# Optimization experiments

Hardware: AMD Instinct MI355X
Metric: run time of the kernel (lower is better)

Reference implementation:

```python
import jax, jax.numpy as jnp
import numpy as np

EPS = 1e-9
# i = 7,6,...,-1 use exp_factor = -(4**i); i = -2 uses 0.0 (matches torch's reversed(range(-2,8)))
EXP_FACTORS = np.array([-(4.0 ** i) for i in range(7, -2, -1)] + [0.0], dtype=np.float32)


def setup_inputs() -> dict:
    key = jax.random.key(0)
    k1, k2 = jax.random.split(key)
    B, N, D = 16, 2048, 3
    preds = jax.random.normal(k1, (B, N, D), dtype=jnp.float32)
    labels = jax.random.normal(k2, (B, N, D), dtype=jnp.float32)
    return {"preds": preds, "labels": labels}


def _pairwise_dist(p1, p2):
    # ||p1||^2 + ||p2||^2 - 2 p1 . p2  -> [B, N, N]
    p1n = jnp.sum(p1 * p1, axis=-1)[..., :, None]
    p2n = jnp.sum(p2 * p2, axis=-1)[..., None, :]
    return p1n + p2n - 2.0 * jnp.einsum('bnd,bmd->bnm', p1, p2)


def _approx_match(pwdist):
    B, N, _ = pwdist.shape
    match0 = jnp.zeros_like(pwdist)
    cost0 = jnp.ones((B, 1, N), dtype=pwdist.dtype)      # per-target remaining capacity
    curr0 = jnp.ones((B, N, 1), dtype=pwdist.dtype)      # per-source remaining currency

    def step(carry, ef):
        match, cost, currency = carry
        bids = jnp.exp(ef * pwdist) * cost
        bids = bids * currency / (jnp.sum(bids, axis=1, keepdims=True) + EPS)
        bid_wt = jnp.minimum(cost / (jnp.sum(bids, axis=1, keepdims=True) + EPS), 1.0)
        bids = bids * bid_wt
        match = match + bids
        cost = jnp.maximum(cost - jnp.sum(bids, axis=1, keepdims=True), 0.0)
        currency = jnp.maximum(currency - jnp.sum(bids, axis=2, keepdims=True), 0.0)
        return (match, cost, currency), None

    (match, _, _), _ = jax.lax.scan(step, (match0, cost0, curr0), jnp.asarray(EXP_FACTORS))
    return match


def reference(preds, labels):
    pwdist = _pairwise_dist(preds, labels)
    match = _approx_match(pwdist)
    return jnp.sum(match * pwdist)
```

## Files before the change

### kernel.cpp

```cpp
#include <hip/hip_runtime.h>
#include <cstddef>

#define BB    16
#define NN    2048
#define BN    (BB * NN)
#define EPSF  1e-9f
#define TPB   512
#define CPT   2
#define SPLIT 16
#define TILE  128
#define CHUNK 1024
#define K9C   4

typedef float v2f __attribute__((ext_vector_type(2)));
typedef float v4f __attribute__((ext_vector_type(4)));

extern "C" __device__ float __ocml_native_exp2_f32(float);
__device__ __forceinline__ float fast_exp2(float x) {
#if __has_builtin(__builtin_amdgcn_exp2f)
    return __builtin_amdgcn_exp2f(x);
#else
    return __ocml_native_exp2_f32(x);
#endif
}

__device__ __forceinline__ v2f pk_fma(v2f a, v2f b, v2f c) {
    v2f d;
    asm("v_pk_fma_f32 %0, %1, %2, %3" : "=v"(d) : "v"(a), "v"(b), "v"(c));
    return d;
}
__device__ __forceinline__ v2f pk_add(v2f a, v2f b) {
    v2f d;
    asm("v_pk_add_f32 %0, %1, %2" : "=v"(d) : "v"(a), "v"(b));
    return d;
}
__device__ __forceinline__ v2f pk_mul(v2f a, v2f b) {
    v2f d;
    asm("v_pk_mul_f32 %0, %1, %2" : "=v"(d) : "v"(a), "v"(b));
    return d;
}

__device__ __forceinline__ float block_sum(float v, int t, float* tmp8) {
#pragma unroll
    for (int o = 32; o > 0; o >>= 1) v += __shfl_down(v, o, 64);
    __syncthreads();
    if ((t & 63) == 0) tmp8[t >> 6] = v;
    __syncthreads();
    float s = 0.0f;
#pragma unroll
    for (int w = 0; w < TPB / 64; w++) s += tmp8[w];
    return s;
}

__global__ __launch_bounds__(TPB, 4) void passA(
    const float* __restrict__ preds, const float* __restrict__ labels,
    const float* __restrict__ curprev, float* __restrict__ curout,
    const float* __restrict__ RSprev, const float* __restrict__ RRprev,
    float* __restrict__ RSz, float* __restrict__ RRz,
    float* __restrict__ Sacc, float* __restrict__ Tacc,
    float* __restrict__ out, float c1, int k)
{
    __shared__ v4f s_pa[TILE / 2];
    __shared__ v4f s_pb[TILE / 2];
    __shared__ v2f s_cu2[TILE / 2];
    __shared__ float s_red[2];
    int blk = blockIdx.x;
    int split = blk & 15, mc = (blk >> 4) & 1, b = blk >> 5;
    int t = threadIdx.x;
    int base = b * NN;

    if (t < TILE) {
        int idx = base + split * TILE + t;
        const float* p = preds + (size_t)idx * 3;
        float px = p[0], py = p[1], pz = p[2];
        float pn = px * px + py * py + pz * pz;
        float cu, contrib = 0.0f;
        if (k == 0) cu = 1.0f;
        else {
            float cup = curprev[idx], rs = RSprev[idx], rr = RRprev[idx];
            contrib = cup * rr;
            cu = fmaxf(cup * (1.0f - rs), 0.0f);
        }
        int h = t >> 1, par = t & 1;
        float* pa = (float*)&s_pa[h];
        float* pb = (float*)&s_pb[h];
        pa[par] = px; pa[2 + par] = py;
        pb[par] = pz; pb[2 + par] = c1 * pn;
        ((float*)s_cu2)[t] = cu;
        if (mc == 0) {
            curout[idx] = cu;
            RSz[idx] = 0.0f; RRz[idx] = 0.0f;
        }
        if (k > 0 && mc == 0) {
#pragma unroll
            for (int o = 32; o > 0; o >>= 1) contrib += __shfl_down(contrib, o, 64);
            if ((t & 63) == 0) s_red[t >> 6] = contrib;
        }
    }

    int m0 = mc * CHUNK + t;
    v2f gx2[CPT], gy2[CPT], gz2[CPT], am2[CPT], Sa2[CPT], Ta2[CPT];
    float n2c1 = -2.0f * c1;
#pragma unroll
    for (int c = 0; c < CPT; c++) {
        int m = m0 + c * TPB;
        const float* l = labels + (size_t)(base + m) * 3;
        float lx = l[0], ly = l[1], lz = l[2];
        float gx = n2c1 * lx, gy = n2c1 * ly, gz = n2c1 * lz;
        float am = c1 * (lx * lx + ly * ly + lz * lz);
        gx2[c] = (v2f){gx, gx}; gy2[c] = (v2f){gy, gy}; gz2[c] = (v2f){gz, gz};
        am2[c] = (v2f){am, am};
        Sa2[c] = (v2f){0.0f, 0.0f}; Ta2[c] = (v2f){0.0f, 0.0f};
    }
    __syncthreads();
    if (k > 0 && mc == 0 && t == 0) atomicAdd(out, s_red[0] + s_red[1]);

#pragma unroll 4
    for (int h = 0; h < TILE / 2; h++) {
        v4f A1 = s_pa[h];
        v4f A2 = s_pb[h];
        v2f cu2 = s_cu2[h];
#pragma unroll
        for (int c = 0; c < CPT; c++) {
            v2f seed = pk_add(A2.zw, am2[c]);
            v2f arg = pk_fma(A1.xy, gx2[c],
                      pk_fma(A1.zw, gy2[c],
                      pk_fma(A2.xy, gz2[c], seed)));
            v2f e2;
            e2.x = fast_exp2(arg.x);
            e2.y = fast_exp2(arg.y);
            Sa2[c] = pk_add(Sa2[c], e2);
            Ta2[c] = pk_fma(e2, cu2, Ta2[c]);
        }
    }
#pragma unroll
    for (int c = 0; c < CPT; c++) {
        int idx = base + m0 + c * TPB;
        atomicAdd(&Sacc[idx], Sa2[c].x + Sa2[c].y);
        atomicAdd(&Tacc[idx], Ta2[c].x + Ta2[c].y);
    }
}

__global__ __launch_bounds__(TPB, 4) void passB(
    const float* __restrict__ preds, const float* __restrict__ labels,
    const float* __restrict__ Sread, const float* __restrict__ Tread,
    const float* __restrict__ costprev, float* __restrict__ costout,
    float* __restrict__ Sz, float* __restrict__ Tz,
    float* __restrict__ RSacc, float* __restrict__ RRacc,
    float c1, float invc1, int k)
{
    __shared__ v4f s_la[TILE / 2];
    __shared__ v4f s_lb[TILE / 2];
    __shared__ v2f s_cc2[TILE / 2];
    int blk = blockIdx.x;
    int split = blk & 15, nc = (blk >> 4) & 1, b = blk >> 5;
    int t = threadIdx.x;
    int base = b * NN;

    if (t < TILE) {
        int idx = base + split * TILE + t;
        const float* l = labels + (size_t)idx * 3;
        float lx = l[0], ly = l[1], lz = l[2];
        float lm2 = lx * lx + ly * ly + lz * lz;
        float S = Sread[idx], T = Tread[idx];
        float cost = (k == 0) ? 1.0f : costprev[idx];
        float D1 = fmaf(cost, S, EPSF);
        float S2 = cost * T / D1;
        float bw = fminf(cost / (S2 + EPSF), 1.0f);
        float cc = cost * bw / D1;
        int h = t >> 1, par = t & 1;
        float* la = (float*)&s_la[h];
        float* lb = (float*)&s_lb[h];
        float n2c1 = -2.0f * c1;
        la[par] = n2c1 * lx; la[2 + par] = n2c1 * ly;
        lb[par] = n2c1 * lz; lb[2 + par] = c1 * lm2;
        ((float*)s_cc2)[t] = cc;
        if (nc == 0) {
            costout[idx] = fmaxf(fmaf(-S2, bw, cost), 0.0f);
            Sz[idx] = 0.0f; Tz[idx] = 0.0f;
        }
    }

    int n0 = nc * CHUNK + t;
    v2f px2[CPT], py2[CPT], pz2[CPT], qq2[CPT], RSa2[CPT], RRa2[CPT];
#pragma unroll
    for (int c = 0; c < CPT; c++) {
        int n = n0 + c * TPB;
        const float* p = preds + (size_t)(base + n) * 3;
        float px = p[0], py = p[1], pz = p[2];
        float qq = c1 * (px * px + py * py + pz * pz);
        px2[c] = (v2f){px, px}; py2[c] = (v2f){py, py}; pz2[c] = (v2f){pz, pz};
        qq2[c] = (v2f){qq, qq};
        RSa2[c] = (v2f){0.0f, 0.0f}; RRa2[c] = (v2f){0.0f, 0.0f};
    }
    __syncthreads();

#pragma unroll 4
    for (int h = 0; h < TILE / 2; h++) {
        v4f L1 = s_la[h];
        v4f L2 = s_lb[h];
        v2f cc2 = s_cc2[h];
#pragma unroll
        for (int c = 0; c < CPT; c++) {
            v2f seed = pk_add(L2.zw, qq2[c]);
            v2f arg = pk_fma(L1.xy, px2[c],
                      pk_fma(L1.zw, py2[c],
                      pk_fma(L2.xy, pz2[c], seed)));
            v2f e2;
            e2.x = fast_exp2(arg.x);
            e2.y = fast_exp2(arg.y);
            v2f w2 = pk_mul(e2, cc2);
            RSa2[c] = pk_add(RSa2[c], w2);
            RRa2[c] = pk_fma(w2, arg, RRa2[c]);
        }
    }
#pragma unroll
    for (int c = 0; c < CPT; c++) {
        int idx = base + n0 + c * TPB;
        atomicAdd(&RSacc[idx], RSa2[c].x + RSa2[c].y);
        atomicAdd(&RRacc[idx], (RRa2[c].x + RRa2[c].y) * invc1);
    }
}

__global__ __launch_bounds__(TPB, 1) void k9(
    const float* __restrict__ preds, const float* __restrict__ labels,
    const float* __restrict__ cur8, const float* __restrict__ RS8,
    const float* __restrict__ RR8, const float* __restrict__ cost9,
    float* __restrict__ out)
{
    __shared__ float tmp8[TPB / 64];
    int b = blockIdx.x, t = threadIdx.x;
    int base = b * NN;

    float cu9[K9C];
    float contrib = 0.0f, csum = 0.0f;
#pragma unroll
    for (int c = 0; c < K9C; c++) {
        int idx = base + t + c * TPB;
        float cup = cur8[idx];
        contrib = fmaf(cup, RR8[idx], contrib);
        float cu = fmaxf(cup * (1.0f - RS8[idx]), 0.0f);
        cu9[c] = cu; csum += cu;
    }
    float contribT = block_sum(contrib, t, tmp8);
    float Cb = block_sum(csum, t, tmp8);

    float A = 0.0f, Bs = 0.0f, Vx = 0.0f, Vy = 0.0f, Vz = 0.0f;
#pragma unroll
    for (int c = 0; c < K9C; c++) {
        int idx = base + t + c * TPB;
        const float* l = labels + (size_t)idx * 3;
        float lx = l[0], ly = l[1], lz = l[2];
        float cost = cost9[idx];
        float D1 = fmaf(cost, 2048.0f, EPSF);
        float S2 = cost * Cb / D1;
        float bw = fminf(cost / (S2 + EPSF), 1.0f);
        float cc = cost * bw / D1;
        A += cc;
        Bs = fmaf(cc, lx * lx + ly * ly + lz * lz, Bs);
        Vx = fmaf(cc, lx, Vx); Vy = fmaf(cc, ly, Vy); Vz = fmaf(cc, lz, Vz);
    }
    float At  = block_sum(A, t, tmp8);
    float Bt  = block_sum(Bs, t, tmp8);
    float Vxt = block_sum(Vx, t, tmp8);
    float Vyt = block_sum(Vy, t, tmp8);
    float Vzt = block_sum(Vz, t, tmp8);

    float acc = 0.0f;
#pragma unroll
    for (int c = 0; c < K9C; c++) {
        int idx = base + t + c * TPB;
        const float* p = preds + (size_t)idx * 3;
        float x = p[0], y = p[1], z = p[2];
        float pn = x * x + y * y + z * z;
        float rr = fmaf(At, pn, Bt) - 2.0f * (x * Vxt + y * Vyt + z * Vzt);
        acc = fmaf(cu9[c], rr, acc);
    }
    float accT = block_sum(acc, t, tmp8);
    if (t == 0) atomicAdd(out, contribT + accT);
}

extern "C" void kernel_launch(void* const* d_in, const int* in_sizes, int n_in,
                              void* d_out, int out_size, void* d_ws, size_t ws_size,
                              hipStream_t stream) {
    const float* preds  = (const float*)d_in[0];
    const float* labels = (const float*)d_in[1];
    float* out = (float*)d_out;
    float* ws  = (float*)d_ws;

    float* S[2]     = {ws + 0 * BN, ws + 2 * BN};
    float* T[2]     = {ws + 1 * BN, ws + 3 * BN};
    float* RS[2]    = {ws + 4 * BN, ws + 6 * BN};
    float* RR[2]    = {ws + 5 * BN, ws + 7 * BN};
    float* curb[2]  = {ws + 8 * BN, ws + 9 * BN};
    float* costb[2] = {ws + 10 * BN, ws + 11 * BN};

    hipMemsetAsync(d_out, 0, sizeof(float), stream);
    hipMemsetAsync(ws, 0, (size_t)2 * BN * sizeof(float), stream);

    static const float efs[9] = {-16384.0f, -4096.0f, -1024.0f, -256.0f, -64.0f,
                                 -16.0f, -4.0f, -1.0f, -0.25f};
    const float log2e = 1.44269504088896f;
    for (int k = 0; k < 9; k++) {
        float c1 = efs[k] * log2e;
        float invc1 = 1.0f / c1;
        int pk = k & 1, pp = (k + 1) & 1;
        passA<<<512, TPB, 0, stream>>>(preds, labels,
            curb[pp], curb[pk],
            RS[pp], RR[pp],
            RS[pk], RR[pk],
            S[pk], T[pk],
            out, c1, k);
        passB<<<512, TPB, 0, stream>>>(preds, labels,
            S[pk], T[pk],
            costb[pk], costb[pp],
            S[pp], T[pp],
            RS[pk], RR[pk],
            c1, invc1, k);
    }
    k9<<<BB, TPB, 0, stream>>>(preds, labels, curb[0], RS[0], RR[0], costb[1], out);
}
```

Before: 308.8 us.

## Split per-point preprocessing into separate kernels, stream packed staging from global memory

```diff
diff --git a/kernel.cpp b/kernel.cpp
--- a/kernel.cpp
+++ b/kernel.cpp
@@ -4,6 +4,7 @@
 #define BB    16
 #define NN    2048
 #define BN    (BB * NN)
+#define PAIRS (BN / 2)
 #define EPSF  1e-9f
 #define TPB   512
 #define CPT   2
@@ -52,51 +53,78 @@
     return s;
 }
 
+__global__ void preA(
+    const float* __restrict__ preds, const float* __restrict__ curprev,
+    const float* __restrict__ RSprev, const float* __restrict__ RRprev,
+    float* __restrict__ curout, float* __restrict__ RSz, float* __restrict__ RRz,
+    v4f* __restrict__ stgA1, v4f* __restrict__ stgA2, v2f* __restrict__ stgAcu,
+    float* __restrict__ out, float c1, int k)
+{
+    __shared__ float tmp8[TPB / 64];
+    int t = threadIdx.x;
+    int idx = blockIdx.x * TPB + t;
+    const float* p = preds + (size_t)idx * 3;
+    float px = p[0], py = p[1], pz = p[2];
+    float pn = px * px + py * py + pz * pz;
+    float cu, contrib = 0.0f;
+    if (k == 0) cu = 1.0f;
+    else {
+        float cup = curprev[idx], rs = RSprev[idx], rr = RRprev[idx];
+        contrib = cup * rr;
+        cu = fmaxf(cup * (1.0f - rs), 0.0f);
+    }
+    curout[idx] = cu;
+    RSz[idx] = 0.0f; RRz[idx] = 0.0f;
+    int h = idx >> 1, par = idx & 1;
+    float* a1 = (float*)&stgA1[h];
+    float* a2 = (float*)&stgA2[h];
+    a1[par] = px;  a1[2 + par] = py;
+    a2[par] = pz;  a2[2 + par] = c1 * pn;
+    ((float*)&stgAcu[h])[par] = cu;
+    if (k > 0) {
+        float s = block_sum(contrib, t, tmp8);
+        if (t == 0) atomicAdd(out, s);
+    }
+}
+
+__global__ void preB(
+    const float* __restrict__ labels, const float* __restrict__ Sread,
+    const float* __restrict__ Tread, const float* __restrict__ costprev,
+    float* __restrict__ costout, float* __restrict__ Sz, float* __restrict__ Tz,
+    v4f* __restrict__ stgB1, v4f* __restrict__ stgB2, v2f* __restrict__ stgBcc,
+    float c1, int k)
+{
+    int idx = blockIdx.x * TPB + threadIdx.x;
+    const float* l = labels + (size_t)idx * 3;
+    float lx = l[0], ly = l[1], lz = l[2];
+    float lm2 = lx * lx + ly * ly + lz * lz;
+    float S = Sread[idx], T = Tread[idx];
+    float cost = (k == 0) ? 1.0f : costprev[idx];
+    float D1 = fmaf(cost, S, EPSF);
+    float S2 = cost * T / D1;
+    float bw = fminf(cost / (S2 + EPSF), 1.0f);
+    float cc = cost * bw / D1;
+    costout[idx] = fmaxf(fmaf(-S2, bw, cost), 0.0f);
+    Sz[idx] = 0.0f; Tz[idx] = 0.0f;
+    int h = idx >> 1, par = idx & 1;
+    float n2c1 = -2.0f * c1;
+    float* b1 = (float*)&stgB1[h];
+    float* b2 = (float*)&stgB2[h];
+    b1[par] = n2c1 * lx;  b1[2 + par] = n2c1 * ly;
+    b2[par] = n2c1 * lz;  b2[2 + par] = c1 * lm2;
+    ((float*)&stgBcc[h])[par] = cc;
+}
+
 __global__ __launch_bounds__(TPB, 4) void passA(
-    const float* __restrict__ preds, const float* __restrict__ labels,
-    const float* __restrict__ curprev, float* __restrict__ curout,
-    const float* __restrict__ RSprev, const float* __restrict__ RRprev,
-    float* __restrict__ RSz, float* __restrict__ RRz,
-    float* __restrict__ Sacc, float* __restrict__ Tacc,
-    float* __restrict__ out, float c1, int k)
-{
-    __shared__ v4f s_pa[TILE / 2];
-    __shared__ v4f s_pb[TILE / 2];
-    __shared__ v2f s_cu2[TILE / 2];
-    __shared__ float s_red[2];
+    const float* __restrict__ labels,
+    const v4f* __restrict__ stgA1, const v4f* __restrict__ stgA2,
+    const v2f* __restrict__ stgAcu,
+    float* __restrict__ Sacc, float* __restrict__ Tacc, float c1)
+{
     int blk = blockIdx.x;
     int split = blk & 15, mc = (blk >> 4) & 1, b = blk >> 5;
     int t = threadIdx.x;
     int base = b * NN;
-
-    if (t < TILE) {
-        int idx = base + split * TILE + t;
-        const float* p = preds + (size_t)idx * 3;
-        float px = p[0], py = p[1], pz = p[2];
-        float pn = px * px + py * py + pz * pz;
-        float cu, contrib = 0.0f;
-        if (k == 0) cu = 1.0f;
-        else {
-            float cup = curprev[idx], rs = RSprev[idx], rr = RRprev[idx];
-            contrib = cup * rr;
-            cu = fmaxf(cup * (1.0f - rs), 0.0f);
-        }
-        int h = t >> 1, par = t & 1;
-        float* pa = (float*)&s_pa[h];
-        float* pb = (float*)&s_pb[h];
-        pa[par] = px; pa[2 + par] = py;
-        pb[par] = pz; pb[2 + par] = c1 * pn;
-        ((float*)s_cu2)[t] = cu;
-        if (mc == 0) {
-            curout[idx] = cu;
-            RSz[idx] = 0.0f; RRz[idx] = 0.0f;
-        }
-        if (k > 0 && mc == 0) {
-#pragma unroll
-            for (int o = 32; o > 0; o >>= 1) contrib += __shfl_down(contrib, o, 64);
-            if ((t & 63) == 0) s_red[t >> 6] = contrib;
-        }
-    }
 
     int m0 = mc * CHUNK + t;
     v2f gx2[CPT], gy2[CPT], gz2[CPT], am2[CPT], Sa2[CPT], Ta2[CPT];
@@ -112,14 +140,13 @@
         am2[c] = (v2f){am, am};
         Sa2[c] = (v2f){0.0f, 0.0f}; Ta2[c] = (v2f){0.0f, 0.0f};
     }
-    __syncthreads();
-    if (k > 0 && mc == 0 && t == 0) atomicAdd(out, s_red[0] + s_red[1]);
-
+
+    int pbase = b * (NN / 2) + split * (TILE / 2);
 #pragma unroll 4
     for (int h = 0; h < TILE / 2; h++) {
-        v4f A1 = s_pa[h];
-        v4f A2 = s_pb[h];
-        v2f cu2 = s_cu2[h];
+        v4f A1 = stgA1[pbase + h];
+        v4f A2 = stgA2[pbase + h];
+        v2f cu2 = stgAcu[pbase + h];
 #pragma unroll
         for (int c = 0; c < CPT; c++) {
             v2f seed = pk_add(A2.zw, am2[c]);
@@ -142,44 +169,16 @@
 }
 
 __global__ __launch_bounds__(TPB, 4) void passB(
-    const float* __restrict__ preds, const float* __restrict__ labels,
-    const float* __restrict__ Sread, const float* __restrict__ Tread,
-    const float* __restrict__ costprev, float* __restrict__ costout,
-    float* __restrict__ Sz, float* __restrict__ Tz,
+    const float* __restrict__ preds,
+    const v4f* __restrict__ stgB1, const v4f* __restrict__ stgB2,
+    const v2f* __restrict__ stgBcc,
     float* __restrict__ RSacc, float* __restrict__ RRacc,
-    float c1, float invc1, int k)
-{
-    __shared__ v4f s_la[TILE / 2];
-    __shared__ v4f s_lb[TILE / 2];
-    __shared__ v2f s_cc2[TILE / 2];
+    float c1, float invc1)
+{
     int blk = blockIdx.x;
     int split = blk & 15, nc = (blk >> 4) & 1, b = blk >> 5;
     int t = threadIdx.x;
     int base = b * NN;
-
-    if (t < TILE) {
-        int idx = base + split * TILE + t;
-        const float* l = labels + (size_t)idx * 3;
-        float lx = l[0], ly = l[1], lz = l[2];
-        float lm2 = lx * lx + ly * ly + lz * lz;
-        float S = Sread[idx], T = Tread[idx];
-        float cost = (k == 0) ? 1.0f : costprev[idx];
-        float D1 = fmaf(cost, S, EPSF);
-        float S2 = cost * T / D1;
-        float bw = fminf(cost / (S2 + EPSF), 1.0f);
-        float cc = cost * bw / D1;
-        int h = t >> 1, par = t & 1;
-        float* la = (float*)&s_la[h];
-        float* lb = (float*)&s_lb[h];
-        float n2c1 = -2.0f * c1;
-        la[par] = n2c1 * lx; la[2 + par] = n2c1 * ly;
-        lb[par] = n2c1 * lz; lb[2 + par] = c1 * lm2;
-        ((float*)s_cc2)[t] = cc;
-        if (nc == 0) {
-            costout[idx] = fmaxf(fmaf(-S2, bw, cost), 0.0f);
-            Sz[idx] = 0.0f; Tz[idx] = 0.0f;
-        }
-    }
 
     int n0 = nc * CHUNK + t;
     v2f px2[CPT], py2[CPT], pz2[CPT], qq2[CPT], RSa2[CPT], RRa2[CPT];
@@ -193,13 +192,13 @@
         qq2[c] = (v2f){qq, qq};
         RSa2[c] = (v2f){0.0f, 0.0f}; RRa2[c] = (v2f){0.0f, 0.0f};
     }
-    __syncthreads();
-
+
+    int pbase = b * (NN / 2) + split * (TILE / 2);
 #pragma unroll 4
     for (int h = 0; h < TILE / 2; h++) {
-        v4f L1 = s_la[h];
-        v4f L2 = s_lb[h];
-        v2f cc2 = s_cc2[h];
+        v4f L1 = stgB1[pbase + h];
+        v4f L2 = stgB2[pbase + h];
+        v2f cc2 = stgBcc[pbase + h];
 #pragma unroll
         for (int c = 0; c < CPT; c++) {
             v2f seed = pk_add(L2.zw, qq2[c]);
@@ -294,6 +293,13 @@
     float* RR[2]    = {ws + 5 * BN, ws + 7 * BN};
     float* curb[2]  = {ws + 8 * BN, ws + 9 * BN};
     float* costb[2] = {ws + 10 * BN, ws + 11 * BN};
+    float* sb = ws + 12 * BN;
+    v4f* stgA1  = (v4f*)sb;
+    v4f* stgA2  = stgA1 + PAIRS;
+    v2f* stgAcu = (v2f*)(stgA2 + PAIRS);
+    v4f* stgB1  = (v4f*)(stgAcu + PAIRS);
+    v4f* stgB2  = stgB1 + PAIRS;
+    v2f* stgBcc = (v2f*)(stgB2 + PAIRS);
 
     hipMemsetAsync(d_out, 0, sizeof(float), stream);
     hipMemsetAsync(ws, 0, (size_t)2 * BN * sizeof(float), stream);
@@ -305,18 +311,21 @@
         float c1 = efs[k] * log2e;
         float invc1 = 1.0f / c1;
         int pk = k & 1, pp = (k + 1) & 1;
-        passA<<<512, TPB, 0, stream>>>(preds, labels,
-            curb[pp], curb[pk],
-            RS[pp], RR[pp],
-            RS[pk], RR[pk],
-            S[pk], T[pk],
-            out, c1, k);
-        passB<<<512, TPB, 0, stream>>>(preds, labels,
+        preA<<<BN / TPB, TPB, 0, stream>>>(preds,
+            curb[pp], RS[pp], RR[pp],
+            curb[pk], RS[pk], RR[pk],
+            stgA1, stgA2, stgAcu, out, c1, k);
+        passA<<<512, TPB, 0, stream>>>(labels,
+            stgA1, stgA2, stgAcu,
+            S[pk], T[pk], c1);
+        preB<<<BN / TPB, TPB, 0, stream>>>(labels,
             S[pk], T[pk],
             costb[pk], costb[pp],
             S[pp], T[pp],
-            RS[pk], RR[pk],
-            c1, invc1, k);
+            stgB1, stgB2, stgBcc, c1, k);
+        passB<<<512, TPB, 0, stream>>>(preds,
+            stgB1, stgB2, stgBcc,
+            RS[pk], RR[pk], c1, invc1);
     }
     k9<<<BB, TPB, 0, stream>>>(preds, labels, curb[0], RS[0], RR[0], costb[1], out);
 }
```

Result: slower. 390.1 us (+26.3%).
